# Performance work log

Hardware: AMD Instinct MI355X
Metric: run time of the kernel (lower is better)

## Reference

```python
import jax, jax.numpy as jnp
import numpy as np

W_BIT = 4
OUT_F = 11008
IN_F = 4096
K = 16
TOKENS = 2048


def unpack_sign(qweight, out_f, in_f):
    """qweight: [w_bit, out_f*in_f//8] ints in [0,256). Each byte packs 8 signs,
    LSB-first: bit j of byte m -> element m*8+j; bit 1 -> +1, bit 0 -> -1.
    Returns float32 signs of shape [w_bit, out_f, in_f]."""
    shifts = jnp.arange(8, dtype=qweight.dtype)
    bits = (qweight[..., None] >> shifts) & 1  # [w_bit, n_bytes, 8]
    sign = (2 * bits - 1).astype(jnp.float32)
    return sign.reshape(qweight.shape[0], out_f, in_f)


def setup_inputs() -> dict:
    key = jax.random.key(0)
    k1, k2, k3, k4 = jax.random.split(key, 4)
    x = jax.random.normal(k1, (TOKENS, IN_F), dtype=jnp.float32)
    qweight = jax.random.randint(k2, (W_BIT, OUT_F * IN_F // 8), 0, 256, dtype=jnp.int32)
    u = jax.random.normal(k3, (W_BIT, OUT_F, K), dtype=jnp.float32) * 0.05
    vt = jax.random.normal(k4, (W_BIT, K, IN_F), dtype=jnp.float32) * 0.05
    return {"x": x, "qweight": qweight, "u": u, "vt": vt}


def reference(x, qweight, u, vt):
    # Reconstruct w = sum_i sign_i * (u_i @ vt_i), then y = x @ w.T  (forward_l0)
    sign = unpack_sign(qweight, OUT_F, IN_F)                  # [b, O, I]
    low_rank = jnp.einsum('bok,bki->boi', u, vt)              # [b, O, I]
    w = jnp.sum(sign * low_rank, axis=0)                      # [O, I]
    return x @ w.T                                            # [T, O]
```

## Files before the change

### kernel.cpp

```cpp
#include <hip/hip_runtime.h>
#include <cstdint>
#include <cstddef>

#define TOKENS 2048
#define IN_F   4096
#define OUT_F  11008
#define W_BIT  4
#define RANK   16
#define QWB    (OUT_F * IN_F / 8)

typedef unsigned short ushort_t;
typedef __attribute__((ext_vector_type(8))) short   short8;
typedef __attribute__((ext_vector_type(4))) float   floatx4;

__device__ __forceinline__ ushort_t f2bf(float f) {
  union { float f; uint32_t u; } c; c.f = f;
  uint32_t r = c.u + 0x7FFFu + ((c.u >> 16) & 1u);
  return (ushort_t)(r >> 16);
}

__device__ __forceinline__ void gl_lds16(const void* g, void* l) {
  __builtin_amdgcn_global_load_lds(
      (const __attribute__((address_space(1))) uint32_t*)g,
      (__attribute__((address_space(3))) uint32_t*)l, 16, 0, 0);
}

__global__ __launch_bounds__(256) void k_cvt_x(const float* __restrict__ x,
                                               ushort_t* __restrict__ xb) {
  int idx = blockIdx.x * 256 + threadIdx.x;
  float4 v = ((const float4*)x)[idx];
  ushort4 r;
  r.x = f2bf(v.x); r.y = f2bf(v.y); r.z = f2bf(v.z); r.w = f2bf(v.w);
  ((ushort4*)xb)[idx] = r;
}

#define N_U  (W_BIT * OUT_F * RANK)
#define N_VT (W_BIT * RANK * IN_F)
__global__ __launch_bounds__(256) void k_prep_uv(const float* __restrict__ u,
                                                 const float* __restrict__ vt,
                                                 ushort_t* __restrict__ ub,
                                                 ushort_t* __restrict__ vtT) {
  int idx = blockIdx.x * 256 + threadIdx.x;
  if (idx < N_U) {
    ub[idx] = f2bf(u[idx]);
  } else {
    int e = idx - N_U;
    int b = e >> 16;
    int r = e & 65535;
    int k = r >> 12;
    int i = r & 4095;
    vtT[((size_t)b * IN_F + i) * RANK + k] = f2bf(vt[e]);
  }
}

__global__ __launch_bounds__(256) void k_build_w(const int* __restrict__ qw,
                                                 const ushort_t* __restrict__ ub,
                                                 const ushort_t* __restrict__ vtT,
                                                 ushort_t* __restrict__ w) {
  __shared__ int qs[W_BIT * 128 * 20];
  const int tid = threadIdx.x;
  const int ob = blockIdx.x / (IN_F / 128);
  const int ib = blockIdx.x % (IN_F / 128);
  const int o0 = ob * 128, i0 = ib * 128;
  const int lane = tid & 63, wv = tid >> 6;
  const int wm = (wv >> 1) * 64, wn = (wv & 1) * 64;
  const int l16 = lane & 15, q = lane >> 4;
  const bool qlo = (q < 2);
  const int koff = (q & 1) * 8;
  const short8 zf = (short8)0;

  #pragma unroll
  for (int n = 0; n < 8; ++n) {
    int c = n * 256 + tid;
    int b = c >> 9, rem = c & 511;
    int row = rem >> 2, part = rem & 3;
    int4 v = *(const int4*)(qw + (size_t)b * QWB +
                            (size_t)(o0 + row) * (IN_F / 8) + (i0 >> 3) + part * 4);
    *(int4*)&qs[(b * 128 + row) * 20 + part * 4] = v;
  }

  floatx4 acc[16];
  #pragma unroll
  for (int i = 0; i < 16; ++i) acc[i] = (floatx4){0.f, 0.f, 0.f, 0.f};

  const int qc_base = (wn >> 3) + (l16 >> 3);
  const int bit = l16 & 7;

  __syncthreads();

  #pragma unroll
  for (int b = 0; b < W_BIT; ++b) {
    short8 af[4], bfr[4];
    #pragma unroll
    for (int mi = 0; mi < 4; ++mi) {
      short8 v = *(const short8*)&ub[((size_t)b * OUT_F + o0 + wm + mi * 16 + l16) * RANK + koff];
      af[mi] = qlo ? v : zf;
    }
    #pragma unroll
    for (int ni = 0; ni < 4; ++ni) {
      short8 v = *(const short8*)&vtT[((size_t)b * IN_F + i0 + wn + ni * 16 + l16) * RANK + koff];
      bfr[ni] = qlo ? v : zf;
    }

    #pragma unroll
    for (int mi = 0; mi < 4; ++mi) {
      floatx4 p[4];
      #pragma unroll
      for (int ni = 0; ni < 4; ++ni)
        p[ni] = __builtin_amdgcn_mfma_f32_16x16x32_bf16(
            af[mi], bfr[ni], (floatx4){0.f, 0.f, 0.f, 0.f}, 0, 0, 0);
      #pragma unroll
      for (int v4 = 0; v4 < 4; ++v4) {
        const int o_loc = wm + mi * 16 + q * 4 + v4;
        const int* qrow = &qs[(b * 128 + o_loc) * 20];
        #pragma unroll
        for (int ni = 0; ni < 4; ++ni) {
          int qv = qrow[qc_base + ni * 2];
          float pv = p[ni][v4];
          acc[mi * 4 + ni][v4] += ((qv >> bit) & 1) ? pv : -pv;
        }
      }
    }
  }

  #pragma unroll
  for (int mi = 0; mi < 4; ++mi) {
    #pragma unroll
    for (int v4 = 0; v4 < 4; ++v4) {
      const int o = o0 + wm + mi * 16 + q * 4 + v4;
      #pragma unroll
      for (int ni = 0; ni < 4; ++ni)
        w[(size_t)o * IN_F + i0 + wn + ni * 16 + l16] = f2bf(acc[mi * 4 + ni][v4]);
    }
  }
}

#define NT (IN_F / 32)
__global__ __launch_bounds__(512) void k_gemm_bt(const ushort_t* __restrict__ A,
                                                 const ushort_t* __restrict__ B,
                                                 float* __restrict__ C) {
  __shared__ __attribute__((aligned(16))) char lds[98304];
  const int tid = threadIdx.x;
  const int wg = (blockIdx.x & 7) * 86 + (blockIdx.x >> 3);
  const int bm = wg & 15;
  const int bn = wg >> 4;
  const int lane = tid & 63, wv = tid >> 6;
  const int wm = wv >> 2, wn = wv & 3;
  const int l16 = lane & 15, q = lane >> 4;
  const int sQ = q ^ ((l16 >> 1) & 3);

  const size_t ar = (size_t)bm * 128, br = (size_t)bn * 256;
  const int qsrc = (tid & 3) ^ ((tid >> 3) & 3);
  const ushort_t* Ae  = A + (ar + (tid >> 2)) * IN_F + qsrc * 8;
  const ushort_t* B0e = B + (br + (tid >> 2)) * IN_F + qsrc * 8;
  const ushort_t* B1e = B + (br + 128 + (tid >> 2)) * IN_F + qsrc * 8;
  char* ldsw = lds + (tid & 448) * 16;
  const int aFrag = (wm * 64 + l16) * 64 + sQ * 16;
  const int bFrag = (wn * 64 + l16) * 64 + sQ * 16;

  floatx4 acc[4][4];
  #pragma unroll
  for (int mi = 0; mi < 4; ++mi)
    #pragma unroll
    for (int ni = 0; ni < 4; ++ni) acc[mi][ni] = (floatx4){0.f, 0.f, 0.f, 0.f};

  short8 a0[4], b0[4], a1[4], b1[4];

#define STAGE(tt) do {                                                       \
    const int _sl = (tt) & 3; const size_t _k0 = (size_t)(tt) * 32;          \
    gl_lds16(Ae + _k0,  ldsw + _sl * 8192);                                  \
    gl_lds16(B0e + _k0, ldsw + 32768 + _sl * 16384);                         \
    gl_lds16(B1e + _k0, ldsw + 32768 + _sl * 16384 + 8192);                  \
  } while (0)

#define LDFRAGS(AF, BF, sl) do {                                             \
    const char* _ab = lds + (sl) * 8192;                                     \
    const char* _bb = lds + 32768 + (sl) * 16384;                            \
    _Pragma("unroll") for (int mi = 0; mi < 4; ++mi)                         \
      AF[mi] = *(const short8*)(_ab + aFrag + mi * 1024);                    \
    _Pragma("unroll") for (int ni = 0; ni < 4; ++ni)                         \
      BF[ni] = *(const short8*)(_bb + bFrag + ni * 1024);                    \
  } while (0)

#define BODY(u, AI, BI, AM, BMr) do {                                        \
    asm volatile("" ::: "memory");                                           \
    __builtin_amdgcn_s_barrier();         \
    asm volatile("" ::: "memory");                                           \
    if ((u) + 3 < NT) STAGE((u) + 3);              \
    if ((u) + 3 < NT)      asm volatile("s_waitcnt vmcnt(6)" ::: "memory");  \
    else if ((u) + 2 < NT) asm volatile("s_waitcnt vmcnt(3)" ::: "memory");  \
    else                   asm volatile("s_waitcnt vmcnt(0)" ::: "memory");  \
    __builtin_amdgcn_s_barrier();            \
    asm volatile("" ::: "memory");                                           \
    LDFRAGS(AI, BI, ((u) + 1) & 3);          \
    __builtin_amdgcn_s_setprio(1);                                           \
    _Pragma("unroll") for (int mi = 0; mi < 4; ++mi)                         \
      _Pragma("unroll") for (int ni = 0; ni < 4; ++ni)                       \
        acc[mi][ni] = __builtin_amdgcn_mfma_f32_16x16x32_bf16(               \
            AM[mi], BMr[ni], acc[mi][ni], 0, 0, 0);                          \
    __builtin_amdgcn_s_setprio(0);                                           \
  } while (0)

  STAGE(0); STAGE(1); STAGE(2);
  asm volatile("s_waitcnt vmcnt(6)" ::: "memory");
  __builtin_amdgcn_s_barrier();
  asm volatile("" ::: "memory");
  LDFRAGS(a0, b0, 0);

  for (int t = 0; t < NT; t += 2) {
    BODY(t,     a1, b1, a0, b0);
    BODY(t + 1, a0, b0, a1, b1);
  }

#undef STAGE
#undef LDFRAGS
#undef BODY

  #pragma unroll
  for (int mi = 0; mi < 4; ++mi) {
    #pragma unroll
    for (int ni = 0; ni < 4; ++ni) {
      #pragma unroll
      for (int v = 0; v < 4; ++v) {
        int r = bm * 128 + wm * 64 + mi * 16 + q * 4 + v;
        int c = bn * 256 + wn * 64 + ni * 16 + l16;
        C[(size_t)r * OUT_F + c] = acc[mi][ni][v];
      }
    }
  }
}

extern "C" void kernel_launch(void* const* d_in, const int* in_sizes, int n_in,
                              void* d_out, int out_size, void* d_ws, size_t ws_size,
                              hipStream_t stream) {
  (void)in_sizes; (void)n_in; (void)out_size; (void)ws_size;
  const float* x  = (const float*)d_in[0];
  const int*   qw = (const int*)d_in[1];
  const float* u  = (const float*)d_in[2];
  const float* vt = (const float*)d_in[3];
  float* out = (float*)d_out;

  char* wsp = (char*)d_ws;
  ushort_t* xb  = (ushort_t*)wsp;
  ushort_t* wb  = (ushort_t*)(wsp + (size_t)TOKENS * IN_F * 2);
  ushort_t* ubf = (ushort_t*)(wsp + (size_t)TOKENS * IN_F * 2 + (size_t)OUT_F * IN_F * 2);
  ushort_t* vtT = (ushort_t*)(wsp + (size_t)TOKENS * IN_F * 2 + (size_t)OUT_F * IN_F * 2 +
                              (size_t)N_U * 2);

  k_cvt_x<<<TOKENS * IN_F / 1024, 256, 0, stream>>>(x, xb);
  k_prep_uv<<<(N_U + N_VT) / 256, 256, 0, stream>>>(u, vt, ubf, vtT);
  k_build_w<<<(OUT_F / 128) * (IN_F / 128), 256, 0, stream>>>(qw, ubf, vtT, wb);
  k_gemm_bt<<<16 * (OUT_F / 256), 512, 0, stream>>>(xb, wb, out);
}
```

Measured before the change: 458.2 us.

## Use 3-slot LDS ring in GEMM and vectorize sign-bit reads in weight build

After: 834.6 us. +82.2%, slower.

```diff
diff --git a/kernel.cpp b/kernel.cpp
--- a/kernel.cpp
+++ b/kernel.cpp
@@ -76,7 +76,8 @@
     int row = rem >> 2, part = rem & 3;
     int4 v = *(const int4*)(qw + (size_t)b * QWB +
                             (size_t)(o0 + row) * (IN_F / 8) + (i0 >> 3) + part * 4);
-    *(int4*)&qs[(b * 128 + row) * 20 + part * 4] = v;
+    int* qrow = &qs[(b * 128 + row) * 20 + (part >> 1) * 8 + (part & 1) * 2];
+    qrow[0] = v.x; qrow[4] = v.y; qrow[1] = v.z; qrow[5] = v.w;
   }
 
   floatx4 acc[16];
@@ -84,6 +85,7 @@
   for (int i = 0; i < 16; ++i) acc[i] = (floatx4){0.f, 0.f, 0.f, 0.f};
 
   const int qc_base = (wn >> 3) + (l16 >> 3);
+  const int qcol = (qc_base & 8) | ((qc_base & 1) << 2);
   const int bit = l16 & 7;
 
   __syncthreads();
@@ -112,10 +114,10 @@
       #pragma unroll
       for (int v4 = 0; v4 < 4; ++v4) {
         const int o_loc = wm + mi * 16 + q * 4 + v4;
-        const int* qrow = &qs[(b * 128 + o_loc) * 20];
+        const int4 qv4 = *(const int4*)&qs[(b * 128 + o_loc) * 20 + qcol];
         #pragma unroll
         for (int ni = 0; ni < 4; ++ni) {
-          int qv = qrow[qc_base + ni * 2];
+          int qv = (ni == 0) ? qv4.x : (ni == 1) ? qv4.y : (ni == 2) ? qv4.z : qv4.w;
           float pv = p[ni][v4];
           acc[mi * 4 + ni][v4] += ((qv >> bit) & 1) ? pv : -pv;
         }
@@ -136,10 +138,11 @@
 }
 
 #define NT (IN_F / 32)
-__global__ __launch_bounds__(512) void k_gemm_bt(const ushort_t* __restrict__ A,
-                                                 const ushort_t* __restrict__ B,
-                                                 float* __restrict__ C) {
-  __shared__ __attribute__((aligned(16))) char lds[98304];
+#define SLOT_BYTES 24576
+__global__ __launch_bounds__(512, 4) void k_gemm_bt(const ushort_t* __restrict__ A,
+                                                    const ushort_t* __restrict__ B,
+                                                    float* __restrict__ C) {
+  __shared__ __attribute__((aligned(16))) char lds[3 * SLOT_BYTES];
   const int tid = threadIdx.x;
   const int wg = (blockIdx.x & 7) * 86 + (blockIdx.x >> 3);
   const int bm = wg & 15;
@@ -154,7 +157,7 @@
   const ushort_t* Ae  = A + (ar + (tid >> 2)) * IN_F + qsrc * 8;
   const ushort_t* B0e = B + (br + (tid >> 2)) * IN_F + qsrc * 8;
   const ushort_t* B1e = B + (br + 128 + (tid >> 2)) * IN_F + qsrc * 8;
-  char* ldsw = lds + (tid & 448) * 16;
+  const int ldsoff = (tid & 448) * 16;
   const int aFrag = (wm * 64 + l16) * 64 + sQ * 16;
   const int bFrag = (wn * 64 + l16) * 64 + sQ * 16;
 
@@ -165,17 +168,19 @@
     for (int ni = 0; ni < 4; ++ni) acc[mi][ni] = (floatx4){0.f, 0.f, 0.f, 0.f};
 
   short8 a0[4], b0[4], a1[4], b1[4];
-
-#define STAGE(tt) do {                                                       \
-    const int _sl = (tt) & 3; const size_t _k0 = (size_t)(tt) * 32;          \
-    gl_lds16(Ae + _k0,  ldsw + _sl * 8192);                                  \
-    gl_lds16(B0e + _k0, ldsw + 32768 + _sl * 16384);                         \
-    gl_lds16(B1e + _k0, ldsw + 32768 + _sl * 16384 + 8192);                  \
+  int sC = 0, sA = SLOT_BYTES, sB = 2 * SLOT_BYTES;
+
+#define STAGE(tt, sb) do {                                                   \
+    const size_t _k0 = (size_t)(tt) * 32;                                    \
+    char* _d = lds + (sb) + ldsoff;                                          \
+    gl_lds16(Ae + _k0,  _d);                                                 \
+    gl_lds16(B0e + _k0, _d + 8192);                                          \
+    gl_lds16(B1e + _k0, _d + 16384);                                         \
   } while (0)
 
-#define LDFRAGS(AF, BF, sl) do {                                             \
-    const char* _ab = lds + (sl) * 8192;                                     \
-    const char* _bb = lds + 32768 + (sl) * 16384;                            \
+#define LDFRAGS(AF, BF, sa) do {                                             \
+    const char* _ab = lds + (sa);                                            \
+    const char* _bb = _ab + 8192;                                            \
     _Pragma("unroll") for (int mi = 0; mi < 4; ++mi)                         \
       AF[mi] = *(const short8*)(_ab + aFrag + mi * 1024);                    \
     _Pragma("unroll") for (int ni = 0; ni < 4; ++ni)                         \
@@ -186,13 +191,15 @@
     asm volatile("" ::: "memory");                                           \
     __builtin_amdgcn_s_barrier();         \
     asm volatile("" ::: "memory");                                           \
-    if ((u) + 3 < NT) STAGE((u) + 3);              \
-    if ((u) + 3 < NT)      asm volatile("s_waitcnt vmcnt(6)" ::: "memory");  \
-    else if ((u) + 2 < NT) asm volatile("s_waitcnt vmcnt(3)" ::: "memory");  \
-    else                   asm volatile("s_waitcnt vmcnt(0)" ::: "memory");  \
+    if ((u) + 2 < NT) {                                                      \
+      STAGE((u) + 2, sB);                    \
+      asm volatile("s_waitcnt vmcnt(3)" ::: "memory");     \
+    } else {                                                                 \
+      asm volatile("s_waitcnt vmcnt(0)" ::: "memory");                       \
+    }                                                                        \
     __builtin_amdgcn_s_barrier();            \
     asm volatile("" ::: "memory");                                           \
-    LDFRAGS(AI, BI, ((u) + 1) & 3);          \
+    LDFRAGS(AI, BI, sA);                     \
     __builtin_amdgcn_s_setprio(1);                                           \
     _Pragma("unroll") for (int mi = 0; mi < 4; ++mi)                         \
       _Pragma("unroll") for (int ni = 0; ni < 4; ++ni)                       \
@@ -201,20 +208,25 @@
     __builtin_amdgcn_s_setprio(0);                                           \
   } while (0)
 
-  STAGE(0); STAGE(1); STAGE(2);
-  asm volatile("s_waitcnt vmcnt(6)" ::: "memory");
+#define ROTATE() do { int _t = sC; sC = sA; sA = sB; sB = _t; } while (0)
+
+  STAGE(0, sC); STAGE(1, sA);
+  asm volatile("s_waitcnt vmcnt(3)" ::: "memory");
   __builtin_amdgcn_s_barrier();
   asm volatile("" ::: "memory");
-  LDFRAGS(a0, b0, 0);
+  LDFRAGS(a0, b0, sC);
 
   for (int t = 0; t < NT; t += 2) {
     BODY(t,     a1, b1, a0, b0);
+    ROTATE();
     BODY(t + 1, a0, b0, a1, b1);
+    ROTATE();
   }
 
 #undef STAGE
 #undef LDFRAGS
 #undef BODY
+#undef ROTATE
 
   #pragma unroll
   for (int mi = 0; mi < 4; ++mi) {
```

## Use six-slot LDS ring with single barrier per k-step in GEMM

Applied to the files above, without the earlier changes.

Result: faster. 428.3 us (-6.5%).

```diff
diff --git a/kernel.cpp b/kernel.cpp
--- a/kernel.cpp
+++ b/kernel.cpp
@@ -135,11 +135,13 @@
   }
 }
 
-#define NT (IN_F / 32)
+#define NSTEP (IN_F / 32)
+#define SLOT  24576
+#define NSLOT 6
 __global__ __launch_bounds__(512) void k_gemm_bt(const ushort_t* __restrict__ A,
                                                  const ushort_t* __restrict__ B,
                                                  float* __restrict__ C) {
-  __shared__ __attribute__((aligned(16))) char lds[98304];
+  __shared__ __attribute__((aligned(16))) char lds[NSLOT * SLOT];
   const int tid = threadIdx.x;
   const int wg = (blockIdx.x & 7) * 86 + (blockIdx.x >> 3);
   const int bm = wg & 15;
@@ -154,7 +156,7 @@
   const ushort_t* Ae  = A + (ar + (tid >> 2)) * IN_F + qsrc * 8;
   const ushort_t* B0e = B + (br + (tid >> 2)) * IN_F + qsrc * 8;
   const ushort_t* B1e = B + (br + 128 + (tid >> 2)) * IN_F + qsrc * 8;
-  char* ldsw = lds + (tid & 448) * 16;
+  const int ldsoff = (tid & 448) * 16;
   const int aFrag = (wm * 64 + l16) * 64 + sQ * 16;
   const int bFrag = (wn * 64 + l16) * 64 + sQ * 16;
 
@@ -164,57 +166,67 @@
     #pragma unroll
     for (int ni = 0; ni < 4; ++ni) acc[mi][ni] = (floatx4){0.f, 0.f, 0.f, 0.f};
 
-  short8 a0[4], b0[4], a1[4], b1[4];
-
-#define STAGE(tt) do {                                                       \
-    const int _sl = (tt) & 3; const size_t _k0 = (size_t)(tt) * 32;          \
-    gl_lds16(Ae + _k0,  ldsw + _sl * 8192);                                  \
-    gl_lds16(B0e + _k0, ldsw + 32768 + _sl * 16384);                         \
-    gl_lds16(B1e + _k0, ldsw + 32768 + _sl * 16384 + 8192);                  \
-  } while (0)
-
-#define LDFRAGS(AF, BF, sl) do {                                             \
-    const char* _ab = lds + (sl) * 8192;                                     \
-    const char* _bb = lds + 32768 + (sl) * 16384;                            \
+  short8 fa0[4], fb0[4], fa1[4], fb1[4];
+  int sLd = SLOT;
+  int sWr = 4 * SLOT;
+
+#define STAGEK(kt, off) do {                                                 \
+    const size_t _k0 = (size_t)(kt) * 32;                                    \
+    char* _d = lds + (off) + ldsoff;                                         \
+    gl_lds16(Ae + _k0,  _d);                                                 \
+    gl_lds16(B0e + _k0, _d + 8192);                                          \
+    gl_lds16(B1e + _k0, _d + 16384);                                         \
+  } while (0)
+
+#define LDFR(FA, FB, off) do {                                               \
+    const char* _ab = lds + (off);                                           \
+    const char* _bb = _ab + 8192;                                            \
     _Pragma("unroll") for (int mi = 0; mi < 4; ++mi)                         \
-      AF[mi] = *(const short8*)(_ab + aFrag + mi * 1024);                    \
+      FA[mi] = *(const short8*)(_ab + aFrag + mi * 1024);                    \
     _Pragma("unroll") for (int ni = 0; ni < 4; ++ni)                         \
-      BF[ni] = *(const short8*)(_bb + bFrag + ni * 1024);                    \
-  } while (0)
-
-#define BODY(u, AI, BI, AM, BMr) do {                                        \
-    asm volatile("" ::: "memory");                                           \
-    __builtin_amdgcn_s_barrier();         \
-    asm volatile("" ::: "memory");                                           \
-    if ((u) + 3 < NT) STAGE((u) + 3);              \
-    if ((u) + 3 < NT)      asm volatile("s_waitcnt vmcnt(6)" ::: "memory");  \
-    else if ((u) + 2 < NT) asm volatile("s_waitcnt vmcnt(3)" ::: "memory");  \
-    else                   asm volatile("s_waitcnt vmcnt(0)" ::: "memory");  \
-    __builtin_amdgcn_s_barrier();            \
-    asm volatile("" ::: "memory");                                           \
-    LDFRAGS(AI, BI, ((u) + 1) & 3);          \
+      FB[ni] = *(const short8*)(_bb + bFrag + ni * 1024);                    \
+  } while (0)
+
+#define MFMA16(MA, MB) do {                                                  \
     __builtin_amdgcn_s_setprio(1);                                           \
     _Pragma("unroll") for (int mi = 0; mi < 4; ++mi)                         \
       _Pragma("unroll") for (int ni = 0; ni < 4; ++ni)                       \
         acc[mi][ni] = __builtin_amdgcn_mfma_f32_16x16x32_bf16(               \
-            AM[mi], BMr[ni], acc[mi][ni], 0, 0, 0);                          \
+            MA[mi], MB[ni], acc[mi][ni], 0, 0, 0);                           \
     __builtin_amdgcn_s_setprio(0);                                           \
   } while (0)
 
-  STAGE(0); STAGE(1); STAGE(2);
-  asm volatile("s_waitcnt vmcnt(6)" ::: "memory");
+#define PHASE(u_, VM, DO_STAGE, FA, FB, MA, MB) do {                         \
+    asm volatile(VM ::: "memory");                                           \
+    __builtin_amdgcn_s_barrier();                                            \
+    asm volatile("" ::: "memory");                                           \
+    LDFR(FA, FB, sLd);                      \
+    if (DO_STAGE) STAGEK((u_) + 4, sWr);                                     \
+    MFMA16(MA, MB);                        \
+    sLd += SLOT; if (sLd == NSLOT * SLOT) sLd = 0;                           \
+    sWr += SLOT; if (sWr == NSLOT * SLOT) sWr = 0;                           \
+  } while (0)
+
+  #pragma unroll
+  for (int p = 0; p < 4; ++p) STAGEK(p, p * SLOT);
+  asm volatile("s_waitcnt vmcnt(9)" ::: "memory");
   __builtin_amdgcn_s_barrier();
   asm volatile("" ::: "memory");
-  LDFRAGS(a0, b0, 0);
-
-  for (int t = 0; t < NT; t += 2) {
-    BODY(t,     a1, b1, a0, b0);
-    BODY(t + 1, a0, b0, a1, b1);
-  }
-
-#undef STAGE
-#undef LDFRAGS
-#undef BODY
+  LDFR(fa0, fb0, 0);
+
+  for (int u = 0; u < NSTEP - 4; u += 2) {
+    PHASE(u,     "s_waitcnt vmcnt(6)", true, fa1, fb1, fa0, fb0);
+    PHASE(u + 1, "s_waitcnt vmcnt(6)", true, fa0, fb0, fa1, fb1);
+  }
+  PHASE(NSTEP - 4, "s_waitcnt vmcnt(6)", false, fa1, fb1, fa0, fb0);
+  PHASE(NSTEP - 3, "s_waitcnt vmcnt(3)", false, fa0, fb0, fa1, fb1);
+  PHASE(NSTEP - 2, "s_waitcnt vmcnt(0)", false, fa1, fb1, fa0, fb0);
+  MFMA16(fa1, fb1);
+
+#undef STAGEK
+#undef LDFR
+#undef MFMA16
+#undef PHASE
 
   #pragma unroll
   for (int mi = 0; mi < 4; ++mi) {
```
